# Kernel optimization log

Hardware: AMD Instinct MI355X
Metric: run time of the kernel (lower is better)

Reference implementation:

```python
import jax, jax.numpy as jnp
import numpy as np

NUM_HEADS = 4
KERNEL_SIZE = 7
DILATION = 1


def setup_inputs() -> dict:
    key = jax.random.key(0)
    ks = jax.random.split(key, 5)
    B, C, H, W = 8, 128, 112, 112
    x = jax.random.normal(ks[0], (B, C, H, W), dtype=jnp.float32)
    qkv_w = jax.random.normal(ks[1], (3 * C, C), dtype=jnp.float32) * 0.02
    qkv_b = jnp.zeros((3 * C,), dtype=jnp.float32)
    rpb = jax.random.normal(ks[2], (NUM_HEADS, 1, 1, KERNEL_SIZE, KERNEL_SIZE), dtype=jnp.float32) * 0.02
    proj_w = jax.random.normal(ks[3], (C, C), dtype=jnp.float32) * 0.02
    proj_b = jnp.zeros((C,), dtype=jnp.float32)
    return {"x": x, "qkv_w": qkv_w, "qkv_b": qkv_b, "rpb": rpb,
            "proj_w": proj_w, "proj_b": proj_b}


def reference(x, qkv_w, qkv_b, rpb, proj_w, proj_b):
    B, C, H, W = x.shape
    nh, ksz, dil = NUM_HEADS, KERNEL_SIZE, DILATION
    hd = C // nh
    scale = hd ** (-0.5)
    # (B,C,H,W) -> (B,H,W,C); no padding needed since H,W >= kernel_size*dilation
    xp = jnp.transpose(x, (0, 2, 3, 1))
    qkv = xp @ qkv_w.T + qkv_b                              # (B,H,W,3C)
    qkv = qkv.reshape(B, H, W, 3, nh, hd).transpose(3, 0, 4, 1, 2, 5)  # (3,B,nh,H,W,hd)
    q = qkv[0] * scale
    k = qkv[1]
    v = qkv[2]
    # q and k are rolled by the same shift, so (q_shift*k_shift).sum = roll of (q*k).sum
    dot = jnp.sum(q * k, axis=-1)                           # (B,nh,H,W)
    attn_cols = []
    for i in range(ksz):
        for j in range(ksz):
            a = jnp.roll(dot, (-i * dil, -j * dil), axis=(2, 3))
            a = a + rpb[:, 0, 0, i, j][:, None, None]       # broadcast (nh,1,1) over (B,nh,H,W)
            attn_cols.append(a)
    attn = jax.nn.softmax(jnp.stack(attn_cols, axis=-1), axis=-1)  # (B,nh,H,W,ks^2)
    out = jnp.zeros_like(v)
    for i in range(ksz):
        for j in range(ksz):
            out = out + attn[..., i * ksz + j, None] * jnp.roll(v, (-i * dil, -j * dil), axis=(2, 3))
    out = out.transpose(0, 2, 3, 1, 4).reshape(B, H, W, C)  # merge heads
    out = out @ proj_w.T + proj_b
    return jnp.transpose(out, (0, 3, 1, 2))                 # (B,C,H,W)
```

## Files before the change

kernel.cpp:

```cpp
#include <hip/hip_runtime.h>

#define B_   8
#define H_   112
#define W_   112
#define HW_  12544
#define C_   128
#define NH_  4
#define HD_  32
#define KK_  49
#define N_   100352
#define SCALE_ 0.17677669529663687f

typedef __attribute__((ext_vector_type(4))) float floatx4;
typedef __attribute__((ext_vector_type(4))) _Float16 halfx4;
typedef __attribute__((ext_vector_type(8))) _Float16 half8;

__global__ __launch_bounds__(256) void k_wt(
    const float* __restrict__ qw, const float* __restrict__ pw,
    _Float16* __restrict__ qwf, _Float16* __restrict__ pwf)
{
  const int idx = blockIdx.x * 256 + threadIdx.x;
  if (idx < 384 * 128) qwf[idx] = (_Float16)qw[idx];
  if (idx < 128 * 128) pwf[idx] = (_Float16)pw[idx];
}

__global__ __launch_bounds__(256, 2) void k_qkv(
    const float* __restrict__ x, const _Float16* __restrict__ qwf,
    const float* __restrict__ qb,
    _Float16* __restrict__ vbuf, float* __restrict__ dotbuf)
{
  __shared__ __align__(16) _Float16 xf[64 * 136];
  const int tid = threadIdx.x;
  const int b   = blockIdx.x / 196;
  const int hw0 = (blockIdx.x % 196) * 64;

  {
    const float* xb = x + (size_t)b * C_ * HW_ + hw0;
    const int p4 = (tid & 15) * 4;
#pragma unroll
    for (int rep = 0; rep < 4; ++rep) {
      const int c = ((tid >> 4) + rep * 16) * 2;
      const float4 fa = *(const float4*)(xb + (size_t)c * HW_ + p4);
      const float4 fb = *(const float4*)(xb + (size_t)(c + 1) * HW_ + p4);
      const float va[4] = {fa.x, fa.y, fa.z, fa.w};
      const float vb[4] = {fb.x, fb.y, fb.z, fb.w};
#pragma unroll
      for (int i = 0; i < 4; ++i) {
        union { _Float16 h[2]; unsigned u; } pk;
        pk.h[0] = (_Float16)va[i];
        pk.h[1] = (_Float16)vb[i];
        *(unsigned*)(xf + (p4 + i) * 136 + c) = pk.u;
      }
    }
  }
  __syncthreads();

  const int w    = __builtin_amdgcn_readfirstlane(tid >> 6);
  const int l    = tid & 63;
  const int m16  = l & 15;
  const int quad = l >> 4;

  int ocbase[6];
#pragma unroll
  for (int g = 0; g < 6; ++g) ocbase[g] = (g >> 1) * 128 + w * 32 + (g & 1) * 16;

  floatx4 acc[6][4];
#pragma unroll
  for (int g = 0; g < 6; ++g)
#pragma unroll
    for (int p = 0; p < 4; ++p) acc[g][p] = (floatx4){0.f, 0.f, 0.f, 0.f};

  for (int ks = 0; ks < 4; ++ks) {
    half8 bb[4];
#pragma unroll
    for (int p = 0; p < 4; ++p) {
      const int off = (p * 16 + m16) * 136 + ks * 32 + quad * 8;
      bb[p] = *(const half8*)(xf + off);
    }
#pragma unroll
    for (int g = 0; g < 6; ++g) {
      const size_t woff = (size_t)(ocbase[g] + m16) * C_ + ks * 32 + quad * 8;
      const half8 wa = *(const half8*)(qwf + woff);
#pragma unroll
      for (int p = 0; p < 4; ++p) {
        acc[g][p] = __builtin_amdgcn_mfma_f32_16x16x32_f16(wa, bb[p], acc[g][p], 0, 0, 0);
      }
    }
  }

  float bias[6][4];
#pragma unroll
  for (int g = 0; g < 6; ++g)
#pragma unroll
    for (int r = 0; r < 4; ++r) bias[g][r] = qb[ocbase[g] + quad * 4 + r];

  const size_t dbase = (size_t)(b * NH_ + w) * HW_ + hw0;

#pragma unroll
  for (int p = 0; p < 4; ++p) {
    float part = 0.f;
#pragma unroll
    for (int t = 0; t < 2; ++t)
#pragma unroll
      for (int r = 0; r < 4; ++r)
        part += (acc[t][p][r] + bias[t][r]) * (acc[2 + t][p][r] + bias[2 + t][r]);
    part += __shfl_xor(part, 16);
    part += __shfl_xor(part, 32);
    if (l < 16) dotbuf[dbase + p * 16 + l] = part * SCALE_;
  }

#pragma unroll
  for (int t = 0; t < 2; ++t) {
#pragma unroll
    for (int p = 0; p < 4; ++p) {
      halfx4 hv;
#pragma unroll
      for (int r = 0; r < 4; ++r) hv[r] = (_Float16)(acc[4 + t][p][r] + bias[4 + t][r]);
      _Float16* vp = vbuf + (dbase + p * 16 + m16) * HD_ + t * 16 + quad * 4;
      *(halfx4*)vp = hv;
    }
  }
}

__global__ __launch_bounds__(256) void k_attn(
    const _Float16* __restrict__ vbuf, const float* __restrict__ dotbuf,
    const float* __restrict__ rpb, _Float16* __restrict__ aof)
{
  __shared__ __align__(16) float at[KK_ * 256];
  __shared__ float rsum[256];
  const int tid  = threadIdx.x;
  const int blk  = ((int)blockIdx.x & 7) * 196 + ((int)blockIdx.x >> 3);
  const int head = blk / 392;
  const int rem  = blk % 392;
  const int b    = rem / 49;
  const int t49  = rem % 49;
  const int r0 = (t49 / 7) * 16;
  const int w0 = (t49 % 7) * 16;
  const float* dptr = dotbuf + (size_t)(b * NH_ + head) * HW_;

  {
    const int r = tid >> 4, wv = tid & 15;
    const int gh = r0 + r, gw = w0 + wv;
    float logit[KK_];
    float m = -1e30f;
#pragma unroll
    for (int i = 0; i < 7; ++i) {
      int hr = gh + i; if (hr >= H_) hr -= H_;
      const float* drow = dptr + hr * W_;
#pragma unroll
      for (int j = 0; j < 7; ++j) {
        int wc = gw + j; if (wc >= W_) wc -= W_;
        const float l = drow[wc] + rpb[head * KK_ + i * 7 + j];
        logit[i * 7 + j] = l;
        m = fmaxf(m, l);
      }
    }
    float s = 0.f;
#pragma unroll
    for (int o = 0; o < KK_; ++o) {
      const float e = __expf(logit[o] - m);
      s += e;
      at[o * 256 + tid] = e;
    }
    rsum[tid] = 1.0f / s;
  }
  __syncthreads();

  const int c4  = tid & 7;
  const int seg = tid >> 3;
  const int r   = seg >> 1;
  const int sx  = (seg & 1) * 8;
  const int gh  = r0 + r;
  const int pxb = r * 16 + sx;
  const _Float16* vb = vbuf + (size_t)(b * NH_ + head) * HW_ * HD_ + c4 * 4;

  float4 acc[8];
#pragma unroll
  for (int xx = 0; xx < 8; ++xx) acc[xx] = make_float4(0.f, 0.f, 0.f, 0.f);

  for (int i = 0; i < 7; ++i) {
    int hr = gh + i; if (hr >= H_) hr -= H_;
    float4 win[14];
#pragma unroll
    for (int t = 0; t < 14; ++t) {
      int wc = w0 + sx + t; if (wc >= W_) wc -= W_;
      const halfx4 hv = *(const halfx4*)(vb + ((size_t)hr * W_ + wc) * HD_);
      win[t] = make_float4((float)hv[0], (float)hv[1], (float)hv[2], (float)hv[3]);
    }
#pragma unroll
    for (int j = 0; j < 7; ++j) {
      const float* arow = at + (i * 7 + j) * 256 + pxb;
      const float4 a0 = *(const float4*)arow;
      const float4 a1 = *(const float4*)(arow + 4);
      const float aw[8] = {a0.x, a0.y, a0.z, a0.w, a1.x, a1.y, a1.z, a1.w};
#pragma unroll
      for (int xx = 0; xx < 8; ++xx) {
        acc[xx].x = fmaf(aw[xx], win[xx + j].x, acc[xx].x);
        acc[xx].y = fmaf(aw[xx], win[xx + j].y, acc[xx].y);
        acc[xx].z = fmaf(aw[xx], win[xx + j].z, acc[xx].z);
        acc[xx].w = fmaf(aw[xx], win[xx + j].w, acc[xx].w);
      }
    }
  }

  const size_t obase =
      ((size_t)b * HW_ + (size_t)gh * W_ + (w0 + sx)) * C_ + head * HD_ + c4 * 4;
#pragma unroll
  for (int xx = 0; xx < 8; ++xx) {
    const float rs = rsum[pxb + xx];
    halfx4 hv;
    hv[0] = (_Float16)(acc[xx].x * rs);
    hv[1] = (_Float16)(acc[xx].y * rs);
    hv[2] = (_Float16)(acc[xx].z * rs);
    hv[3] = (_Float16)(acc[xx].w * rs);
    *(halfx4*)(aof + obase + (size_t)xx * C_) = hv;
  }
}

__global__ __launch_bounds__(256, 2) void k_proj(
    const _Float16* __restrict__ aof, const _Float16* __restrict__ pwf,
    const float* __restrict__ pb, float* __restrict__ out)
{
  const int tid = threadIdx.x;
  const int b   = blockIdx.x / 196;
  const int hw0 = (blockIdx.x % 196) * 64;
  const int w    = __builtin_amdgcn_readfirstlane(tid >> 6);
  const int l    = tid & 63;
  const int m16  = l & 15;
  const int quad = l >> 4;

  floatx4 acc[2][4];
#pragma unroll
  for (int t = 0; t < 2; ++t)
#pragma unroll
    for (int p = 0; p < 4; ++p) acc[t][p] = (floatx4){0.f, 0.f, 0.f, 0.f};

  const size_t pxbase = (size_t)b * HW_ + hw0;

  for (int ks = 0; ks < 4; ++ks) {
    half8 bb[4];
#pragma unroll
    for (int p = 0; p < 4; ++p) {
      const size_t off = (pxbase + p * 16 + m16) * C_ + ks * 32 + quad * 8;
      bb[p] = *(const half8*)(aof + off);
    }
#pragma unroll
    for (int t = 0; t < 2; ++t) {
      const size_t woff = (size_t)(w * 32 + t * 16 + m16) * C_ + ks * 32 + quad * 8;
      const half8 wa = *(const half8*)(pwf + woff);
#pragma unroll
      for (int p = 0; p < 4; ++p) {
        acc[t][p] = __builtin_amdgcn_mfma_f32_16x16x32_f16(wa, bb[p], acc[t][p], 0, 0, 0);
      }
    }
  }

#pragma unroll
  for (int t = 0; t < 2; ++t) {
    float bias[4];
#pragma unroll
    for (int r = 0; r < 4; ++r) bias[r] = pb[w * 32 + t * 16 + quad * 4 + r];
#pragma unroll
    for (int p = 0; p < 4; ++p) {
#pragma unroll
      for (int r = 0; r < 4; ++r) {
        const int oc = w * 32 + t * 16 + quad * 4 + r;
        out[(size_t)b * C_ * HW_ + (size_t)oc * HW_ + hw0 + p * 16 + m16] =
            acc[t][p][r] + bias[r];
      }
    }
  }
}

extern "C" void kernel_launch(void* const* d_in, const int* in_sizes, int n_in,
                              void* d_out, int out_size, void* d_ws, size_t ws_size,
                              hipStream_t stream) {
  const float* x   = (const float*)d_in[0];
  const float* qw  = (const float*)d_in[1];
  const float* qb  = (const float*)d_in[2];
  const float* rpb = (const float*)d_in[3];
  const float* pw  = (const float*)d_in[4];
  const float* pb  = (const float*)d_in[5];
  float* out = (float*)d_out;

  _Float16* vbuf = (_Float16*)d_ws;
  float* dotb = (float*)(vbuf + (size_t)N_ * C_);
  _Float16* aof = (_Float16*)(dotb + (size_t)N_ * NH_);
  _Float16* qwf = aof + (size_t)N_ * C_;
  _Float16* pwf = qwf + 384 * C_;

  hipLaunchKernelGGL(k_wt,   dim3(192), dim3(256), 0, stream, qw, pw, qwf, pwf);
  hipLaunchKernelGGL(k_qkv,  dim3(N_ / 64), dim3(256), 0, stream, x, qwf, qb, vbuf, dotb);
  hipLaunchKernelGGL(k_attn, dim3(NH_ * B_ * 49), dim3(256), 0, stream, vbuf, dotb, rpb, aof);
  hipLaunchKernelGGL(k_proj, dim3(N_ / 64), dim3(256), 0, stream, aof, pwf, pb, out);
}
```

Measured before the change: 185.7 us.

## Split QKV projection across 8 waves with LDS reduction of q·k partials

The QKV kernel now runs 512 threads per block, so each wave computes half of a head's 32 channels (3x4 accumulators instead of 6x4). This cuts accumulator register pressure and raises the occupancy target. Per-wave partial q·k dot products go into shared memory and are summed by the first 256 threads after an extra barrier. The trade-off is an added sync and extra LDS traffic, plus each wave now reloads the shared x tile for fewer MFMAs.

```diff
diff --git a/kernel.cpp b/kernel.cpp
--- a/kernel.cpp
+++ b/kernel.cpp
@@ -24,12 +24,13 @@
   if (idx < 128 * 128) pwf[idx] = (_Float16)pw[idx];
 }
 
-__global__ __launch_bounds__(256, 2) void k_qkv(
+__global__ __launch_bounds__(512, 4) void k_qkv(
     const float* __restrict__ x, const _Float16* __restrict__ qwf,
     const float* __restrict__ qb,
     _Float16* __restrict__ vbuf, float* __restrict__ dotbuf)
 {
   __shared__ __align__(16) _Float16 xf[64 * 136];
+  __shared__ float dotp[8][64];
   const int tid = threadIdx.x;
   const int b   = blockIdx.x / 196;
   const int hw0 = (blockIdx.x % 196) * 64;
@@ -38,8 +39,8 @@
     const float* xb = x + (size_t)b * C_ * HW_ + hw0;
     const int p4 = (tid & 15) * 4;
 #pragma unroll
-    for (int rep = 0; rep < 4; ++rep) {
-      const int c = ((tid >> 4) + rep * 16) * 2;
+    for (int rep = 0; rep < 2; ++rep) {
+      const int c = ((tid >> 4) + rep * 32) * 2;
       const float4 fa = *(const float4*)(xb + (size_t)c * HW_ + p4);
       const float4 fb = *(const float4*)(xb + (size_t)(c + 1) * HW_ + p4);
       const float va[4] = {fa.x, fa.y, fa.z, fa.w};
@@ -55,18 +56,17 @@
   }
   __syncthreads();
 
-  const int w    = __builtin_amdgcn_readfirstlane(tid >> 6);
+  const int wid  = __builtin_amdgcn_readfirstlane(tid >> 6);
+  const int w    = wid >> 1;
+  const int h    = wid & 1;
   const int l    = tid & 63;
   const int m16  = l & 15;
   const int quad = l >> 4;
-
-  int ocbase[6];
-#pragma unroll
-  for (int g = 0; g < 6; ++g) ocbase[g] = (g >> 1) * 128 + w * 32 + (g & 1) * 16;
-
-  floatx4 acc[6][4];
-#pragma unroll
-  for (int g = 0; g < 6; ++g)
+  const int rowq = w * 32 + h * 16;
+
+  floatx4 acc[3][4];
+#pragma unroll
+  for (int g = 0; g < 3; ++g)
 #pragma unroll
     for (int p = 0; p < 4; ++p) acc[g][p] = (floatx4){0.f, 0.f, 0.f, 0.f};
 
@@ -78,8 +78,8 @@
       bb[p] = *(const half8*)(xf + off);
     }
 #pragma unroll
-    for (int g = 0; g < 6; ++g) {
-      const size_t woff = (size_t)(ocbase[g] + m16) * C_ + ks * 32 + quad * 8;
+    for (int g = 0; g < 3; ++g) {
+      const size_t woff = (size_t)(g * 128 + rowq + m16) * C_ + ks * 32 + quad * 8;
       const half8 wa = *(const half8*)(qwf + woff);
 #pragma unroll
       for (int p = 0; p < 4; ++p) {
@@ -88,37 +88,42 @@
     }
   }
 
-  float bias[6][4];
-#pragma unroll
-  for (int g = 0; g < 6; ++g)
-#pragma unroll
-    for (int r = 0; r < 4; ++r) bias[g][r] = qb[ocbase[g] + quad * 4 + r];
+  float bq[4], bk[4], bv[4];
+#pragma unroll
+  for (int r = 0; r < 4; ++r) {
+    bq[r] = qb[rowq + quad * 4 + r];
+    bk[r] = qb[128 + rowq + quad * 4 + r];
+    bv[r] = qb[256 + rowq + quad * 4 + r];
+  }
 
   const size_t dbase = (size_t)(b * NH_ + w) * HW_ + hw0;
+
+#pragma unroll
+  for (int p = 0; p < 4; ++p) {
+    halfx4 hv;
+#pragma unroll
+    for (int r = 0; r < 4; ++r) hv[r] = (_Float16)(acc[2][p][r] + bv[r]);
+    _Float16* vp = vbuf + (dbase + p * 16 + m16) * HD_ + h * 16 + quad * 4;
+    *(halfx4*)vp = hv;
+  }
 
 #pragma unroll
   for (int p = 0; p < 4; ++p) {
     float part = 0.f;
 #pragma unroll
-    for (int t = 0; t < 2; ++t)
-#pragma unroll
-      for (int r = 0; r < 4; ++r)
-        part += (acc[t][p][r] + bias[t][r]) * (acc[2 + t][p][r] + bias[2 + t][r]);
+    for (int r = 0; r < 4; ++r)
+      part += (acc[0][p][r] + bq[r]) * (acc[1][p][r] + bk[r]);
     part += __shfl_xor(part, 16);
     part += __shfl_xor(part, 32);
-    if (l < 16) dotbuf[dbase + p * 16 + l] = part * SCALE_;
-  }
-
-#pragma unroll
-  for (int t = 0; t < 2; ++t) {
-#pragma unroll
-    for (int p = 0; p < 4; ++p) {
-      halfx4 hv;
-#pragma unroll
-      for (int r = 0; r < 4; ++r) hv[r] = (_Float16)(acc[4 + t][p][r] + bias[4 + t][r]);
-      _Float16* vp = vbuf + (dbase + p * 16 + m16) * HD_ + t * 16 + quad * 4;
-      *(halfx4*)vp = hv;
-    }
+    if (l < 16) dotp[wid][p * 16 + l] = part;
+  }
+  __syncthreads();
+
+  if (tid < 256) {
+    const int w2 = tid >> 6;
+    const int l2 = tid & 63;
+    const float s = dotp[w2 * 2][l2] + dotp[w2 * 2 + 1][l2];
+    dotbuf[(size_t)(b * NH_ + w2) * HW_ + hw0 + l2] = s * SCALE_;
   }
 }
 
@@ -290,7 +295,7 @@
   _Float16* pwf = qwf + 384 * C_;
 
   hipLaunchKernelGGL(k_wt,   dim3(192), dim3(256), 0, stream, qw, pw, qwf, pwf);
-  hipLaunchKernelGGL(k_qkv,  dim3(N_ / 64), dim3(256), 0, stream, x, qwf, qb, vbuf, dotb);
+  hipLaunchKernelGGL(k_qkv,  dim3(N_ / 64), dim3(512), 0, stream, x, qwf, qb, vbuf, dotb);
   hipLaunchKernelGGL(k_attn, dim3(NH_ * B_ * 49), dim3(256), 0, stream, vbuf, dotb, rpb, aof);
   hipLaunchKernelGGL(k_proj, dim3(N_ / 64), dim3(256), 0, stream, aof, pwf, pb, out);
 }
```

After: 184.0 us. No clear change (-1.0%).
